# Kernel tuning notes

Measured on AMD Instinct MI355X. Metric: run time of the kernel, lower is better.

Reference implementation:

```python
import jax, jax.numpy as jnp
import numpy as np
import math

D_MODEL = 256
D_STATE = 16
D_CONV = 4
EXPAND = 2
D_INNER = EXPAND * D_MODEL          # 512
DT_RANK = math.ceil(D_MODEL / 16)   # 16
EPS = 1e-5


def rmsnorm(x, w):
    return x * jax.lax.rsqrt(jnp.mean(x * x, axis=-1, keepdims=True) + EPS) * w


def mamba_mixer(x, in_proj, conv_w, conv_b, x_proj, dt_w, dt_b, A_log, Dp, out_proj):
    # x: [B, L, d_model]
    Bsz, L, _ = x.shape
    xz = x @ in_proj.T                       # [B, L, 2*d_inner]
    xh, z = jnp.split(xz, 2, axis=-1)        # each [B, L, d_inner]
    # causal depthwise conv1d over time (d_conv=4)
    xp = jnp.pad(xh, ((0, 0), (D_CONV - 1, 0), (0, 0)))
    xc = sum(xp[:, k:k + L, :] * conv_w[:, k] for k in range(D_CONV)) + conv_b
    xc = jax.nn.silu(xc)                     # [B, L, d_inner]
    x_dbl = xc @ x_proj.T                    # [B, L, dt_rank + 2*d_state]
    dt, Bm, Cm = jnp.split(x_dbl, [DT_RANK, DT_RANK + D_STATE], axis=-1)
    delta = jax.nn.softplus(dt @ dt_w.T + dt_b)   # [B, L, d_inner]
    A = -jnp.exp(A_log)                      # [d_inner, d_state]
    dA = jnp.exp(jnp.einsum('bld,dn->lbdn', delta, A))        # [L,B,d,n]
    dBu = jnp.einsum('bld,bln,bld->lbdn', delta, Bm, xc)       # [L,B,d,n]

    def step(h, inp):
        a, b = inp
        h = a * h + b
        return h, h

    h0 = jnp.zeros((Bsz, D_INNER, D_STATE), xc.dtype)
    _, hs = jax.lax.scan(step, h0, (dA, dBu))                  # [L,B,d,n]
    y = jnp.einsum('lbdn,bln->bld', hs, Cm) + xc * Dp          # [B,L,d_inner]
    y = y * jax.nn.silu(z)
    return y @ out_proj.T                                      # [B,L,d_model]


def block(x, norm_w, in_proj, conv_w, conv_b, x_proj, dt_w, dt_b, A_log, Dp, out_proj):
    # Block with fused_add_norm=False, residual=None: residual = x, h = mixer(norm(x))
    residual = x
    h = mamba_mixer(rmsnorm(x, norm_w), in_proj, conv_w, conv_b, x_proj,
                    dt_w, dt_b, A_log, Dp, out_proj)
    return h + residual


def setup_inputs() -> dict:
    key = jax.random.key(0)
    ks = jax.random.split(key, 16)
    B, L = 4, 2048

    def n(k, shape, s=0.02):
        return jax.random.normal(k, shape, jnp.float32) * s

    inp = {"x": jax.random.normal(ks[0], (B, L, D_MODEL), jnp.float32)}
    i = 1
    for pre in ("fw", "bw"):
        inp[pre + "_norm"] = jnp.ones((D_MODEL,), jnp.float32)
        inp[pre + "_in_proj"] = n(ks[i], (2 * D_INNER, D_MODEL)); i += 1
        inp[pre + "_conv_w"] = n(ks[i], (D_INNER, D_CONV), 0.1); i += 1
        inp[pre + "_conv_b"] = jnp.zeros((D_INNER,), jnp.float32)
        inp[pre + "_x_proj"] = n(ks[i], (DT_RANK + 2 * D_STATE, D_INNER)); i += 1
        inp[pre + "_dt_w"] = n(ks[i], (D_INNER, DT_RANK), 0.1); i += 1
        inp[pre + "_dt_b"] = n(ks[i], (D_INNER,), 0.1); i += 1
        inp[pre + "_A_log"] = jnp.log(jnp.tile(jnp.arange(1, D_STATE + 1, dtype=jnp.float32), (D_INNER, 1)))
        inp[pre + "_D"] = jnp.ones((D_INNER,), jnp.float32)
        inp[pre + "_out_proj"] = n(ks[i], (D_MODEL, D_INNER)); i += 1
    return inp


def reference(x,
              fw_norm, fw_in_proj, fw_conv_w, fw_conv_b, fw_x_proj, fw_dt_w, fw_dt_b, fw_A_log, fw_D, fw_out_proj,
              bw_norm, bw_in_proj, bw_conv_w, bw_conv_b, bw_x_proj, bw_dt_w, bw_dt_b, bw_A_log, bw_D, bw_out_proj):
    fwd = block(x, fw_norm, fw_in_proj, fw_conv_w, fw_conv_b, fw_x_proj,
                fw_dt_w, fw_dt_b, fw_A_log, fw_D, fw_out_proj)
    xb = jnp.flip(x, axis=1)
    bwd = block(xb, bw_norm, bw_in_proj, bw_conv_w, bw_conv_b, bw_x_proj,
                bw_dt_w, bw_dt_b, bw_A_log, bw_D, bw_out_proj)
    bwd = jnp.flip(bwd, axis=1)
    return fwd + bwd
```

## Files before the change

### kernel.cpp

```cpp
#include <hip/hip_runtime.h>
#include <hip/hip_bf16.h>
#include <math.h>


#define NTOK 8192
#define LL   2048
#define DM   256
#define DI   512
#define DS2  16
#define CL   64
#define NCH  32
#define PLANE 65536
#define KSTEP 64

typedef __bf16 bf16x8 __attribute__((ext_vector_type(8)));
typedef float f32x4 __attribute__((ext_vector_type(4)));

__device__ inline unsigned short f2bf(float f) {
    unsigned u = __float_as_uint(f);
    unsigned r = (u + 0x7fffu + ((u >> 16) & 1u)) >> 16;
    return (unsigned short)r;
}
__device__ inline float bf2f(unsigned short s) {
    return __uint_as_float((unsigned)s << 16);
}

#define L2E 1.4426950408889634f
#define LN2 0.6931471805599453f

__device__ inline float softplus_fast(float x) {
    float e = __builtin_amdgcn_exp2f(-fabsf(x) * L2E);
    float l = __builtin_amdgcn_logf(1.f + e);
    return fmaxf(x, 0.f) + l * LN2;
}

__device__ inline int xcd_swz(int bid, int nwg) {
    int q = nwg >> 3, r = nwg & 7;
    int xcd = bid & 7, lo = bid >> 3;
    return (xcd < r ? xcd * (q + 1) : r * (q + 1) + (xcd - r) * q) + lo;
}

#define GLDS(gp, lp) __builtin_amdgcn_global_load_lds( \
    (const __attribute__((address_space(1))) void*)(gp), \
    (__attribute__((address_space(3))) void*)(lp), 16, 0, 0)

__global__ __launch_bounds__(256) void prep_kernel(
    const float* __restrict__ ip0, const float* __restrict__ nw0,
    const float* __restrict__ ip1, const float* __restrict__ nw1,
    const float* __restrict__ xp0, const float* __restrict__ dtw0,
    const float* __restrict__ xp1, const float* __restrict__ dtw1,
    const float* __restrict__ op0, const float* __restrict__ op1,
    unsigned short* __restrict__ w_in, unsigned short* __restrict__ w_p2,
    unsigned short* __restrict__ w_out,
    const float* __restrict__ x, unsigned short* __restrict__ xn) {
    int bid = blockIdx.x, tid = threadIdx.x;
    if (bid < 2048) {
        int dir = bid >> 10, n = bid & 1023;
        const float* ip = dir ? ip1 : ip0;
        const float* nw = dir ? nw1 : nw0;
        w_in[(size_t)bid * 256 + tid] = f2bf(ip[n * 256 + tid] * nw[tid]);
    } else if (bid < 3200) {
        int idx = bid - 2048;
        int dir = idx / 576, row = idx % 576;
        const float* xp = dir ? xp1 : xp0;
        const float* dtw = dir ? dtw1 : dtw0;
        unsigned short* dst = w_p2 + (size_t)idx * 512;
        for (int k = tid; k < 512; k += 256) {
            float v = 0.f;
            if (row < 512) {
                #pragma unroll
                for (int r = 0; r < 16; ++r) v = fmaf(dtw[row * 16 + r], xp[r * 512 + k], v);
            } else if (row < 544) {
                v = xp[(16 + row - 512) * 512 + k];
            }
            dst[k] = f2bf(v);
        }
    } else if (bid < 3456) {
        int n = bid - 3200;
        for (int k = tid; k < 1024; k += 256) {
            float v = (k < 512) ? op0[n * 512 + k] : op1[n * 512 + (k - 512)];
            w_out[(size_t)n * 1024 + k] = f2bf(v);
        }
    } else {
        int t = bid - 3456;
        float v = x[(size_t)t * DM + tid];
        float ss = v * v;
        #pragma unroll
        for (int m = 1; m < 64; m <<= 1) ss += __shfl_xor(ss, m);
        __shared__ float ws[4];
        if ((tid & 63) == 0) ws[tid >> 6] = ss;
        __syncthreads();
        float tot = ws[0] + ws[1] + ws[2] + ws[3];
        float scale = rsqrtf(tot / (float)DM + 1e-5f);
        xn[(size_t)t * DM + tid] = f2bf(v * scale);
    }
}

#define EPI_IN  0
#define EPI_P2  1
#define EPI_OUT 2

template <int EPI>
__global__ __launch_bounds__(256) void mfma_gemm(
    const unsigned short* __restrict__ A0, const unsigned short* __restrict__ A1,
    const unsigned short* __restrict__ Wb, int K,
    unsigned short* __restrict__ d0, unsigned short* __restrict__ d1,
    unsigned short* __restrict__ e0, unsigned short* __restrict__ e1,
    const float* __restrict__ aux0, const float* __restrict__ aux1,
    const float* __restrict__ Xres, float* __restrict__ outF) {
    __shared__ char lds[2][2][8192];
    int tid = threadIdx.x;
    int lane = tid & 63, wid = tid >> 6;
    int wm = wid >> 1, wn = wid & 1;
    int nwg = gridDim.x * gridDim.y;
    int lid = xcd_swz(blockIdx.y * gridDim.x + blockIdx.x, nwg);
    int n0 = (lid % gridDim.x) * 64;
    int m0 = (lid / gridDim.x) * 64;
    int dir = blockIdx.z;
    const unsigned short* A = dir ? A1 : A0;
    const unsigned short* W = Wb + ((EPI == EPI_P2) ? (size_t)dir * 576 * 512 : 0);

    const int s1 = tid, s2 = tid + 256;
    const int r1 = s1 >> 3, c1 = (s1 & 7) ^ (r1 & 7);
    const int r2 = s2 >> 3, c2 = (s2 & 7) ^ (r2 & 7);

    f32x4 acc[2][2] = {};
    int nt = K / KSTEP;

    auto stage = [&](int t, int buf) {
        int k0 = t * KSTEP;
        GLDS(A + (size_t)(m0 + r1) * K + k0 + c1 * 8, &lds[buf][0][0] + wid * 1024);
        GLDS(A + (size_t)(m0 + r2) * K + k0 + c2 * 8, &lds[buf][0][0] + 4096 + wid * 1024);
        GLDS(W + (size_t)(n0 + r1) * K + k0 + c1 * 8, &lds[buf][1][0] + wid * 1024);
        GLDS(W + (size_t)(n0 + r2) * K + k0 + c2 * 8, &lds[buf][1][0] + 4096 + wid * 1024);
    };

    stage(0, 0);
    for (int t = 0; t < nt; ++t) {
        int buf = t & 1;
        __syncthreads();
        if (t + 1 < nt) stage(t + 1, buf ^ 1);
        const char* Ab = &lds[buf][0][0];
        const char* Bb = &lds[buf][1][0];
        bf16x8 af[2][2], bfv[2][2];
        #pragma unroll
        for (int mf = 0; mf < 2; ++mf)
            #pragma unroll
            for (int kf = 0; kf < 2; ++kf) {
                int r = wm * 32 + mf * 16 + (lane & 15);
                int c = (lane >> 4) + kf * 4;
                af[mf][kf] = *(const bf16x8*)(Ab + r * 128 + ((c ^ (r & 7)) << 4));
            }
        #pragma unroll
        for (int nf = 0; nf < 2; ++nf)
            #pragma unroll
            for (int kf = 0; kf < 2; ++kf) {
                int r = wn * 32 + nf * 16 + (lane & 15);
                int c = (lane >> 4) + kf * 4;
                bfv[nf][kf] = *(const bf16x8*)(Bb + r * 128 + ((c ^ (r & 7)) << 4));
            }
        #pragma unroll
        for (int kf = 0; kf < 2; ++kf)
            #pragma unroll
            for (int mf = 0; mf < 2; ++mf)
                #pragma unroll
                for (int nf = 0; nf < 2; ++nf)
                    acc[mf][nf] = __builtin_amdgcn_mfma_f32_16x16x32_bf16(
                        af[mf][kf], bfv[nf][kf], acc[mf][nf], 0, 0, 0);
    }

    int cb0 = n0 + wn * 32 + (lane & 15);
    int rb0 = m0 + wm * 32 + ((lane >> 4) << 2);
    #pragma unroll
    for (int mf = 0; mf < 2; ++mf)
        #pragma unroll
        for (int nf = 0; nf < 2; ++nf) {
            int n = cb0 + nf * 16;
            #pragma unroll
            for (int r = 0; r < 4; ++r) {
                int m = rb0 + mf * 16 + r;
                float v = acc[mf][nf][r];
                if (EPI == EPI_IN) {
                    d0[(size_t)m * 2048 + n] = f2bf(v);
                } else if (EPI == EPI_P2) {
                    if (n < 512) {
                        float sv = v + (dir ? aux1 : aux0)[n];
                        (dir ? d1 : d0)[(size_t)m * 512 + n] = f2bf(softplus_fast(sv));
                    } else if (n < 544) {
                        (dir ? e1 : e0)[(size_t)m * 32 + (n - 512)] = f2bf(v);
                    }
                } else {
                    outF[(size_t)m * 256 + n] = v + 2.f * Xres[(size_t)m * 256 + n];
                }
            }
        }
}

__global__ __launch_bounds__(256) void conv_silu_kernel(
    const unsigned short* __restrict__ xz,
    const float* __restrict__ cw0, const float* __restrict__ cw1,
    const float* __restrict__ cb0, const float* __restrict__ cb1,
    unsigned short* __restrict__ o0, unsigned short* __restrict__ o1) {
    int dir = blockIdx.y;
    const float* cw = dir ? cw1 : cw0;
    const float* cb = dir ? cb1 : cb0;
    unsigned short* xc = dir ? o1 : o0;
    int idx8 = blockIdx.x * 256 + threadIdx.x;
    int t = idx8 >> 6;
    int c8 = (idx8 & 63) << 3;
    int l = t & (LL - 1);
    const unsigned short* xh = xz + (size_t)dir * 1024 + c8;

    float wreg[32];
    #pragma unroll
    for (int q = 0; q < 8; ++q)
        *(float4*)&wreg[q * 4] = *(const float4*)&cw[c8 * 4 + q * 4];
    float acc[8];
    *(float4*)&acc[0] = *(const float4*)&cb[c8];
    *(float4*)&acc[4] = *(const float4*)&cb[c8 + 4];

    #pragma unroll
    for (int k = 0; k < 4; ++k) {
        int lo = dir ? (l + 3 - k) : (l - 3 + k);
        if (lo < 0 || lo >= LL) continue;
        uint4 u = *(const uint4*)(xh + (size_t)(t + lo - l) * 2048);
        unsigned wv[4] = {u.x, u.y, u.z, u.w};
        #pragma unroll
        for (int j = 0; j < 4; ++j) {
            float flo = __uint_as_float(wv[j] << 16);
            float fhi = __uint_as_float(wv[j] & 0xffff0000u);
            acc[2 * j]     = fmaf(flo, wreg[(2 * j) * 4 + k], acc[2 * j]);
            acc[2 * j + 1] = fmaf(fhi, wreg[(2 * j + 1) * 4 + k], acc[2 * j + 1]);
        }
    }
    unsigned out[4];
    #pragma unroll
    for (int j = 0; j < 4; ++j) {
        float a0 = acc[2 * j], a1 = acc[2 * j + 1];
        float s0 = a0 / (1.f + __expf(-a0));
        float s1 = a1 / (1.f + __expf(-a1));
        out[j] = (unsigned)f2bf(s0) | ((unsigned)f2bf(s1) << 16);
    }
    *(uint4*)(xc + (size_t)idx8 * 8) = make_uint4(out[0], out[1], out[2], out[3]);
}

__global__ __launch_bounds__(256, 4) void scan_part1(
    const unsigned short* __restrict__ dlt0, const unsigned short* __restrict__ dlt1,
    const unsigned short* __restrict__ xc0, const unsigned short* __restrict__ xc1,
    const unsigned short* __restrict__ bc0, const unsigned short* __restrict__ bc1,
    const float* __restrict__ Al0, const float* __restrict__ Al1,
    const float* __restrict__ Dp0, const float* __restrict__ Dp1,
    float* __restrict__ AC, float* __restrict__ HC,
    unsigned* __restrict__ yls0, unsigned* __restrict__ yls1) {
    int dir = blockIdx.z;
    const unsigned short* delta = dir ? dlt1 : dlt0;
    const unsigned short* xc    = dir ? xc1 : xc0;
    const unsigned short* bc    = dir ? bc1 : bc0;
    const float* Alog           = dir ? Al1 : Al0;
    const float* Dp             = dir ? Dp1 : Dp0;
    unsigned* yls               = dir ? yls1 : yls0;
    int b = blockIdx.y >> 5, ch = blockIdx.y & 31;
    int d0 = blockIdx.x * 128;
    int tid = threadIdx.x;
    int dg = tid >> 1, nq = tid & 1;
    int d = d0 + dg;

    __shared__ unsigned sdxu[CL][128];
    __shared__ unsigned sBC[CL][16];
    {
        int row = tid >> 2, q = tid & 3;
        int lr = ch * CL + row;
        int l = dir ? (LL - 1 - lr) : lr;
        size_t t = (size_t)b * LL + l;
        const uint4* dp = (const uint4*)(delta + t * DI + d0 + q * 32);
        const uint4* xp = (const uint4*)(xc + t * DI + d0 + q * 32);
        #pragma unroll
        for (int hh = 0; hh < 4; ++hh) {
            uint4 du = dp[hh], xu = xp[hh];
            unsigned dw[4] = {du.x, du.y, du.z, du.w};
            unsigned xw[4] = {xu.x, xu.y, xu.z, xu.w};
            #pragma unroll
            for (int j = 0; j < 4; ++j) {
                int col = q * 32 + hh * 8 + 2 * j;
                sdxu[row][col ^ row]       = (dw[j] & 0xffffu) | (xw[j] << 16);
                sdxu[row][(col + 1) ^ row] = (dw[j] >> 16) | (xw[j] & 0xffff0000u);
            }
        }
        uint2 Bu = *(const uint2*)(bc + t * 32 + q * 4);
        uint2 Cu = *(const uint2*)(bc + t * 32 + 16 + q * 4);
        sBC[row][q * 4 + 0] = (Bu.x & 0xffffu) | (Cu.x << 16);
        sBC[row][q * 4 + 1] = (Bu.x >> 16) | (Cu.x & 0xffff0000u);
        sBC[row][q * 4 + 2] = (Bu.y & 0xffffu) | (Cu.y << 16);
        sBC[row][q * 4 + 3] = (Bu.y >> 16) | (Cu.y & 0xffff0000u);
    }
    __syncthreads();

    float Av[8], Avl[8];
    {
        float4 Ala = *(const float4*)&Alog[d * DS2 + nq * 8];
        float4 Alb = *(const float4*)&Alog[d * DS2 + nq * 8 + 4];
        Av[0] = -__expf(Ala.x); Av[1] = -__expf(Ala.y);
        Av[2] = -__expf(Ala.z); Av[3] = -__expf(Ala.w);
        Av[4] = -__expf(Alb.x); Av[5] = -__expf(Alb.y);
        Av[6] = -__expf(Alb.z); Av[7] = -__expf(Alb.w);
    }
    #pragma unroll
    for (int j = 0; j < 8; ++j) Avl[j] = Av[j] * L2E;
    bool fast = true;
    #pragma unroll
    for (int j = 0; j < 7; ++j)
        fast = fast && (fabsf(Av[j + 1] - Av[j] + 1.f) < 1e-2f);

    float Dv = Dp[d];
    float h[8] = {0.f, 0.f, 0.f, 0.f, 0.f, 0.f, 0.f, 0.f};
    float sdl = 0.f;
    const float nL2E = -L2E;

    if (fast) {
        #pragma unroll 2
        for (int r = 0; r < CL; ++r) {
            unsigned u = sdxu[r][dg ^ r];
            float dl = __uint_as_float(u << 16);
            float xcv = __uint_as_float(u & 0xffff0000u);
            uint4 q0 = *(const uint4*)&sBC[r][nq * 8];
            uint4 q1 = *(const uint4*)&sBC[r][nq * 8 + 4];
            unsigned bw[8] = {q0.x, q0.y, q0.z, q0.w, q1.x, q1.y, q1.z, q1.w};
            float u0 = dl * xcv;
            sdl += dl;
            float e  = __builtin_amdgcn_exp2f(dl * Avl[0]);
            float rr = __builtin_amdgcn_exp2f(dl * nL2E);
            float ts = 0.f;
            #pragma unroll
            for (int j = 0; j < 8; ++j) {
                float Bf = __uint_as_float(bw[j] << 16);
                float Cf = __uint_as_float(bw[j] & 0xffff0000u);
                h[j] = fmaf(e, h[j], u0 * Bf);
                ts = fmaf(h[j], Cf, ts);
                if (j < 7) e *= rr;
            }
            ts += __shfl_xor(ts, 1);
            if (nq == 0) {
                int lr = ch * CL + r;
                float yv = fmaf(xcv, Dv, ts);
                yls[((size_t)b * LL + lr) * DI + d] =
                    (unsigned)f2bf(yv) | ((unsigned)f2bf(sdl) << 16);
            }
        }
    } else {
        #pragma unroll 2
        for (int r = 0; r < CL; ++r) {
            unsigned u = sdxu[r][dg ^ r];
            float dl = __uint_as_float(u << 16);
            float xcv = __uint_as_float(u & 0xffff0000u);
            uint4 q0 = *(const uint4*)&sBC[r][nq * 8];
            uint4 q1 = *(const uint4*)&sBC[r][nq * 8 + 4];
            unsigned bw[8] = {q0.x, q0.y, q0.z, q0.w, q1.x, q1.y, q1.z, q1.w};
            float u0 = dl * xcv;
            sdl += dl;
            float ts = 0.f;
            #pragma unroll
            for (int j = 0; j < 8; ++j) {
                float Bf = __uint_as_float(bw[j] << 16);
                float Cf = __uint_as_float(bw[j] & 0xffff0000u);
                float e = __builtin_amdgcn_exp2f(dl * Avl[j]);
                h[j] = fmaf(e, h[j], u0 * Bf);
                ts = fmaf(h[j], Cf, ts);
            }
            ts += __shfl_xor(ts, 1);
            if (nq == 0) {
                int lr = ch * CL + r;
                float yv = fmaf(xcv, Dv, ts);
                yls[((size_t)b * LL + lr) * DI + d] =
                    (unsigned)f2bf(yv) | ((unsigned)f2bf(sdl) << 16);
            }
        }
    }

    size_t base = (size_t)ch * PLANE + (size_t)(((dir * 4 + b) * DI + d) * DS2 + nq * 8);
    float ac[8];
    #pragma unroll
    for (int j = 0; j < 8; ++j) ac[j] = __builtin_amdgcn_exp2f(Avl[j] * sdl);
    *(float4*)&AC[base]     = make_float4(ac[0], ac[1], ac[2], ac[3]);
    *(float4*)&AC[base + 4] = make_float4(ac[4], ac[5], ac[6], ac[7]);
    *(float4*)&HC[base]     = make_float4(h[0], h[1], h[2], h[3]);
    *(float4*)&HC[base + 4] = make_float4(h[4], h[5], h[6], h[7]);
}

__global__ __launch_bounds__(256) void scan_part2(
    const float* __restrict__ AC, const float* __restrict__ HC,
    float* __restrict__ HIN) {
    int idx = blockIdx.x * 256 + threadIdx.x;
    float hin = 0.f;
    #pragma unroll
    for (int ch = 0; ch < NCH; ++ch) {
        size_t o = (size_t)ch * PLANE + idx;
        HIN[o] = hin;
        hin = fmaf(AC[o], hin, HC[o]);
    }
}

__global__ __launch_bounds__(256, 8) void scan_lite(
    const unsigned* __restrict__ yls0, const unsigned* __restrict__ yls1,
    const unsigned short* __restrict__ bc0, const unsigned short* __restrict__ bc1,
    const unsigned short* __restrict__ xz,
    const float* __restrict__ Al0, const float* __restrict__ Al1,
    const float* __restrict__ HIN, unsigned short* __restrict__ ycat) {
    int dir = blockIdx.z;
    const unsigned* yls         = dir ? yls1 : yls0;
    const unsigned short* bc    = dir ? bc1 : bc0;
    const float* Alog           = dir ? Al1 : Al0;
    int b = blockIdx.y >> 5, ch = blockIdx.y & 31;
    int d0 = blockIdx.x * 64;
    int tid = threadIdx.x;
    int dg = tid & 63, lg = tid >> 6;
    int d = d0 + dg;

    __shared__ unsigned sC[CL][8];
    {
        int row = tid >> 2, q = tid & 3;
        if (q < 2) {
            int lr = ch * CL + row;
            int l = dir ? (LL - 1 - lr) : lr;
            size_t t = (size_t)b * LL + l;
            uint4 cu = *(const uint4*)(bc + t * 32 + 16 + q * 8);
            *(uint4*)&sC[row][q * 4] = cu;
        }
    }
    __syncthreads();

    float Av[16];
    bool fastA = true;
    #pragma unroll
    for (int qq = 0; qq < 4; ++qq) {
        float4 Al = *(const float4*)&Alog[d * DS2 + qq * 4];
        Av[qq * 4 + 0] = -__expf(Al.x);
        Av[qq * 4 + 1] = -__expf(Al.y);
        Av[qq * 4 + 2] = -__expf(Al.z);
        Av[qq * 4 + 3] = -__expf(Al.w);
    }
    #pragma unroll
    for (int n = 0; n < 16; ++n)
        fastA = fastA && (fabsf(Av[n] + (float)(n + 1)) < 1e-3f * (float)(n + 1));

    float hin[16];
    size_t hbase = (size_t)ch * PLANE + (size_t)(((dir * 4 + b) * DI + d) * DS2);
    #pragma unroll
    for (int qq = 0; qq < 4; ++qq)
        *(float4*)&hin[qq * 4] = *(const float4*)&HIN[hbase + qq * 4];

    #pragma unroll 2
    for (int i = 0; i < 16; ++i) {
        int row = lg * 16 + i;
        int lr = ch * CL + row;
        int ll = dir ? (LL - 1 - lr) : lr;
        size_t tt = (size_t)b * LL + ll;
        unsigned u = yls[((size_t)b * LL + lr) * DI + d];
        float yv = __uint_as_float(u << 16);
        float s  = __uint_as_float(u & 0xffff0000u);
        if (fastA) {
            float E = __builtin_amdgcn_exp2f(-s * L2E);
            if (__any(E > 3e-6f)) {
                float acc = 0.f;
                #pragma unroll
                for (int p = 7; p >= 0; --p) {
                    unsigned cp = sC[row][p];
                    float C0 = __uint_as_float(cp << 16);
                    float C1 = __uint_as_float(cp & 0xffff0000u);
                    acc = fmaf(acc, E, C1 * hin[2 * p + 1]);
                    acc = fmaf(acc, E, C0 * hin[2 * p]);
                }
                yv = fmaf(acc, E, yv);
            }
        } else {
            float acc = 0.f;
            #pragma unroll
            for (int p = 0; p < 8; ++p) {
                unsigned cp = sC[row][p];
                float C0 = __uint_as_float(cp << 16);
                float C1 = __uint_as_float(cp & 0xffff0000u);
                float e0 = __builtin_amdgcn_exp2f(s * Av[2 * p] * L2E);
                float e1 = __builtin_amdgcn_exp2f(s * Av[2 * p + 1] * L2E);
                acc = fmaf(e0 * hin[2 * p], C0, acc);
                acc = fmaf(e1 * hin[2 * p + 1], C1, acc);
            }
            yv += acc;
        }
        float zz = bf2f(xz[tt * 2048 + (size_t)dir * 1024 + 512 + d]);
        yv *= zz / (1.f + __expf(-zz));
        ycat[tt * 1024 + (size_t)dir * 512 + d] = f2bf(yv);
    }
}

extern "C" void kernel_launch(void* const* d_in, const int* in_sizes, int n_in,
                              void* d_out, int out_size, void* d_ws, size_t ws_size,
                              hipStream_t stream) {
    const float* x = (const float*)d_in[0];
    const float* p[2][10];
    for (int dir = 0; dir < 2; ++dir)
        for (int i = 0; i < 10; ++i)
            p[dir][i] = (const float*)d_in[1 + dir * 10 + i];

    char* w = (char*)d_ws;
    auto alloc = [&](size_t bytes) { char* q = w; w += (bytes + 255) & ~(size_t)255; return q; };
    unsigned short* xn    = (unsigned short*)alloc((size_t)NTOK * DM * 2);
    unsigned short* w_in  = (unsigned short*)alloc((size_t)2048 * 256 * 2);
    unsigned short* w_p2  = (unsigned short*)alloc((size_t)1152 * 512 * 2);
    unsigned short* w_out = (unsigned short*)alloc((size_t)256 * 1024 * 2);
    unsigned short* xzcat = (unsigned short*)alloc((size_t)NTOK * 2048 * 2);
    unsigned short *xcb[2], *dlt[2], *bc[2];
    unsigned* yls[2];
    for (int dir = 0; dir < 2; ++dir) {
        xcb[dir] = (unsigned short*)alloc((size_t)NTOK * DI * 2);
        dlt[dir] = (unsigned short*)alloc((size_t)NTOK * DI * 2);
        bc[dir]  = (unsigned short*)alloc((size_t)NTOK * 32 * 2);
        yls[dir] = (unsigned*)alloc((size_t)NTOK * DI * 4);
    }
    unsigned short* ycat = (unsigned short*)alloc((size_t)NTOK * 1024 * 2);
    float* AC  = (float*)alloc((size_t)NCH * PLANE * 4);
    float* HC  = (float*)alloc((size_t)NCH * PLANE * 4);
    float* HIN = (float*)alloc((size_t)NCH * PLANE * 4);
    float* out = (float*)d_out;

    prep_kernel<<<3456 + NTOK, 256, 0, stream>>>(
        p[0][1], p[0][0], p[1][1], p[1][0],
        p[0][4], p[0][5], p[1][4], p[1][5],
        p[0][9], p[1][9], w_in, w_p2, w_out, x, xn);

    mfma_gemm<EPI_IN><<<dim3(32, 128, 1), 256, 0, stream>>>(
        xn, xn, w_in, 256, xzcat, nullptr, nullptr, nullptr,
        nullptr, nullptr, nullptr, nullptr);

    conv_silu_kernel<<<dim3(2048, 2), 256, 0, stream>>>(
        xzcat, p[0][2], p[1][2], p[0][3], p[1][3], xcb[0], xcb[1]);

    mfma_gemm<EPI_P2><<<dim3(9, 128, 2), 256, 0, stream>>>(
        xcb[0], xcb[1], w_p2, 512, dlt[0], dlt[1], bc[0], bc[1],
        p[0][6], p[1][6], nullptr, nullptr);

    scan_part1<<<dim3(DI / 128, 4 * NCH, 2), 256, 0, stream>>>(
        dlt[0], dlt[1], xcb[0], xcb[1], bc[0], bc[1], p[0][7], p[1][7],
        p[0][8], p[1][8], AC, HC, yls[0], yls[1]);
    scan_part2<<<PLANE / 256, 256, 0, stream>>>(AC, HC, HIN);
    scan_lite<<<dim3(DI / 64, 4 * NCH, 2), 256, 0, stream>>>(
        yls[0], yls[1], bc[0], bc[1], xzcat,
        p[0][7], p[1][7], HIN, ycat);

    mfma_gemm<EPI_OUT><<<dim3(4, 128, 1), 256, 0, stream>>>(
        ycat, ycat, w_out, 1024, nullptr, nullptr, nullptr, nullptr,
        nullptr, nullptr, x, out);
}
```

Before: 169.9 us.

## Enlarge GEMM M-tile to 128, coalesce scan loads, break scan dependency chains

The MFMA GEMM now computes 128x64 tiles instead of 64x64, with each wave owning 64 rows. The grids are halved and __launch_bounds__(256,3) is added, which raises reuse of the W tile but uses more registers and LDS and launches fewer workgroups. The scan_part1 staging loads are reordered so adjacent threads read adjacent 16-byte chunks, and the B/C pack is written as a single uint4 store. The inner scan loop now computes the decay powers with a shallow multiply tree and splits the C-dot accumulation into two chains, shortening serial dependencies.

Measured after the change: 171.8 us. Within noise of the previous version (+1.1%).

```diff
diff --git a/kernel.cpp b/kernel.cpp
--- a/kernel.cpp
+++ b/kernel.cpp
@@ -101,38 +101,43 @@
 #define EPI_OUT 2
 
 template <int EPI>
-__global__ __launch_bounds__(256) void mfma_gemm(
+__global__ __launch_bounds__(256, 3) void mfma_gemm(
     const unsigned short* __restrict__ A0, const unsigned short* __restrict__ A1,
     const unsigned short* __restrict__ Wb, int K,
     unsigned short* __restrict__ d0, unsigned short* __restrict__ d1,
     unsigned short* __restrict__ e0, unsigned short* __restrict__ e1,
     const float* __restrict__ aux0, const float* __restrict__ aux1,
     const float* __restrict__ Xres, float* __restrict__ outF) {
-    __shared__ char lds[2][2][8192];
+    __shared__ char lds[2][24576];
     int tid = threadIdx.x;
     int lane = tid & 63, wid = tid >> 6;
     int wm = wid >> 1, wn = wid & 1;
     int nwg = gridDim.x * gridDim.y;
     int lid = xcd_swz(blockIdx.y * gridDim.x + blockIdx.x, nwg);
     int n0 = (lid % gridDim.x) * 64;
-    int m0 = (lid / gridDim.x) * 64;
+    int m0 = (lid / gridDim.x) * 128;
     int dir = blockIdx.z;
     const unsigned short* A = dir ? A1 : A0;
     const unsigned short* W = Wb + ((EPI == EPI_P2) ? (size_t)dir * 576 * 512 : 0);
 
-    const int s1 = tid, s2 = tid + 256;
-    const int r1 = s1 >> 3, c1 = (s1 & 7) ^ (r1 & 7);
-    const int r2 = s2 >> 3, c2 = (s2 & 7) ^ (r2 & 7);
-
-    f32x4 acc[2][2] = {};
+    f32x4 acc[4][2] = {};
     int nt = K / KSTEP;
 
     auto stage = [&](int t, int buf) {
         int k0 = t * KSTEP;
-        GLDS(A + (size_t)(m0 + r1) * K + k0 + c1 * 8, &lds[buf][0][0] + wid * 1024);
-        GLDS(A + (size_t)(m0 + r2) * K + k0 + c2 * 8, &lds[buf][0][0] + 4096 + wid * 1024);
-        GLDS(W + (size_t)(n0 + r1) * K + k0 + c1 * 8, &lds[buf][1][0] + wid * 1024);
-        GLDS(W + (size_t)(n0 + r2) * K + k0 + c2 * 8, &lds[buf][1][0] + 4096 + wid * 1024);
+        char* base = &lds[buf][0];
+        #pragma unroll
+        for (int i = 0; i < 4; ++i) {
+            int s = i * 256 + tid;
+            int r = s >> 3, cd = (s & 7) ^ (r & 7);
+            GLDS(A + (size_t)(m0 + r) * K + k0 + cd * 8, base + i * 4096 + wid * 1024);
+        }
+        #pragma unroll
+        for (int i = 0; i < 2; ++i) {
+            int s = i * 256 + tid;
+            int r = s >> 3, cd = (s & 7) ^ (r & 7);
+            GLDS(W + (size_t)(n0 + r) * K + k0 + cd * 8, base + 16384 + i * 4096 + wid * 1024);
+        }
     };
 
     stage(0, 0);
@@ -140,14 +145,14 @@
         int buf = t & 1;
         __syncthreads();
         if (t + 1 < nt) stage(t + 1, buf ^ 1);
-        const char* Ab = &lds[buf][0][0];
-        const char* Bb = &lds[buf][1][0];
-        bf16x8 af[2][2], bfv[2][2];
-        #pragma unroll
-        for (int mf = 0; mf < 2; ++mf)
+        const char* Ab = &lds[buf][0];
+        const char* Bb = &lds[buf][16384];
+        bf16x8 af[4][2], bfv[2][2];
+        #pragma unroll
+        for (int mf = 0; mf < 4; ++mf)
             #pragma unroll
             for (int kf = 0; kf < 2; ++kf) {
-                int r = wm * 32 + mf * 16 + (lane & 15);
+                int r = wm * 64 + mf * 16 + (lane & 15);
                 int c = (lane >> 4) + kf * 4;
                 af[mf][kf] = *(const bf16x8*)(Ab + r * 128 + ((c ^ (r & 7)) << 4));
             }
@@ -162,7 +167,7 @@
         #pragma unroll
         for (int kf = 0; kf < 2; ++kf)
             #pragma unroll
-            for (int mf = 0; mf < 2; ++mf)
+            for (int mf = 0; mf < 4; ++mf)
                 #pragma unroll
                 for (int nf = 0; nf < 2; ++nf)
                     acc[mf][nf] = __builtin_amdgcn_mfma_f32_16x16x32_bf16(
@@ -170,9 +175,9 @@
     }
 
     int cb0 = n0 + wn * 32 + (lane & 15);
-    int rb0 = m0 + wm * 32 + ((lane >> 4) << 2);
-    #pragma unroll
-    for (int mf = 0; mf < 2; ++mf)
+    int rb0 = m0 + wm * 64 + ((lane >> 4) << 2);
+    #pragma unroll
+    for (int mf = 0; mf < 4; ++mf)
         #pragma unroll
         for (int nf = 0; nf < 2; ++nf) {
             int n = cb0 + nf * 16;
@@ -272,26 +277,25 @@
         int lr = ch * CL + row;
         int l = dir ? (LL - 1 - lr) : lr;
         size_t t = (size_t)b * LL + l;
-        const uint4* dp = (const uint4*)(delta + t * DI + d0 + q * 32);
-        const uint4* xp = (const uint4*)(xc + t * DI + d0 + q * 32);
+        const uint4* dp = (const uint4*)(delta + t * DI + d0);
+        const uint4* xp = (const uint4*)(xc + t * DI + d0);
         #pragma unroll
         for (int hh = 0; hh < 4; ++hh) {
-            uint4 du = dp[hh], xu = xp[hh];
+            uint4 du = dp[hh * 4 + q], xu = xp[hh * 4 + q];
             unsigned dw[4] = {du.x, du.y, du.z, du.w};
             unsigned xw[4] = {xu.x, xu.y, xu.z, xu.w};
             #pragma unroll
             for (int j = 0; j < 4; ++j) {
-                int col = q * 32 + hh * 8 + 2 * j;
+                int col = hh * 32 + q * 8 + 2 * j;
                 sdxu[row][col ^ row]       = (dw[j] & 0xffffu) | (xw[j] << 16);
                 sdxu[row][(col + 1) ^ row] = (dw[j] >> 16) | (xw[j] & 0xffff0000u);
             }
         }
         uint2 Bu = *(const uint2*)(bc + t * 32 + q * 4);
         uint2 Cu = *(const uint2*)(bc + t * 32 + 16 + q * 4);
-        sBC[row][q * 4 + 0] = (Bu.x & 0xffffu) | (Cu.x << 16);
-        sBC[row][q * 4 + 1] = (Bu.x >> 16) | (Cu.x & 0xffff0000u);
-        sBC[row][q * 4 + 2] = (Bu.y & 0xffffu) | (Cu.y << 16);
-        sBC[row][q * 4 + 3] = (Bu.y >> 16) | (Cu.y & 0xffff0000u);
+        *(uint4*)&sBC[row][q * 4] = make_uint4(
+            (Bu.x & 0xffffu) | (Cu.x << 16), (Bu.x >> 16) | (Cu.x & 0xffff0000u),
+            (Bu.y & 0xffffu) | (Cu.y << 16), (Bu.y >> 16) | (Cu.y & 0xffff0000u));
     }
     __syncthreads();
 
@@ -327,17 +331,24 @@
             unsigned bw[8] = {q0.x, q0.y, q0.z, q0.w, q1.x, q1.y, q1.z, q1.w};
             float u0 = dl * xcv;
             sdl += dl;
-            float e  = __builtin_amdgcn_exp2f(dl * Avl[0]);
+            float e0 = __builtin_amdgcn_exp2f(dl * Avl[0]);
             float rr = __builtin_amdgcn_exp2f(dl * nL2E);
-            float ts = 0.f;
+            float rr2 = rr * rr, rr4 = rr2 * rr2;
+            float e[8];
+            e[0] = e0;        e[1] = e0 * rr;
+            e[2] = e0 * rr2;  e[3] = e[1] * rr2;
+            e[4] = e0 * rr4;  e[5] = e[1] * rr4;
+            e[6] = e[2] * rr4; e[7] = e[3] * rr4;
+            float tsa = 0.f, tsb = 0.f;
             #pragma unroll
             for (int j = 0; j < 8; ++j) {
                 float Bf = __uint_as_float(bw[j] << 16);
                 float Cf = __uint_as_float(bw[j] & 0xffff0000u);
-                h[j] = fmaf(e, h[j], u0 * Bf);
-                ts = fmaf(h[j], Cf, ts);
-                if (j < 7) e *= rr;
-            }
+                h[j] = fmaf(e[j], h[j], u0 * Bf);
+                if (j & 1) tsb = fmaf(h[j], Cf, tsb);
+                else       tsa = fmaf(h[j], Cf, tsa);
+            }
+            float ts = tsa + tsb;
             ts += __shfl_xor(ts, 1);
             if (nq == 0) {
                 int lr = ch * CL + r;
@@ -526,14 +537,14 @@
         p[0][4], p[0][5], p[1][4], p[1][5],
         p[0][9], p[1][9], w_in, w_p2, w_out, x, xn);
 
-    mfma_gemm<EPI_IN><<<dim3(32, 128, 1), 256, 0, stream>>>(
+    mfma_gemm<EPI_IN><<<dim3(32, 64, 1), 256, 0, stream>>>(
         xn, xn, w_in, 256, xzcat, nullptr, nullptr, nullptr,
         nullptr, nullptr, nullptr, nullptr);
 
     conv_silu_kernel<<<dim3(2048, 2), 256, 0, stream>>>(
         xzcat, p[0][2], p[1][2], p[0][3], p[1][3], xcb[0], xcb[1]);
 
-    mfma_gemm<EPI_P2><<<dim3(9, 128, 2), 256, 0, stream>>>(
+    mfma_gemm<EPI_P2><<<dim3(9, 64, 2), 256, 0, stream>>>(
         xcb[0], xcb[1], w_p2, 512, dlt[0], dlt[1], bc[0], bc[1],
         p[0][6], p[1][6], nullptr, nullptr);
 
@@ -545,7 +556,7 @@
         yls[0], yls[1], bc[0], bc[1], xzcat,
         p[0][7], p[1][7], HIN, ycat);
 
-    mfma_gemm<EPI_OUT><<<dim3(4, 128, 1), 256, 0, stream>>>(
+    mfma_gemm<EPI_OUT><<<dim3(4, 64, 1), 256, 0, stream>>>(
         ycat, ycat, w_out, 1024, nullptr, nullptr, nullptr, nullptr,
         nullptr, nullptr, x, out);
 }
```
